# Performance work log

Measured on AMD Instinct MI355X. Metric: run time of the kernel, lower is better.

The kernel has to match this reference:

```python
import jax, jax.numpy as jnp
import numpy as np

N, K, H = 98, 10, 4        # landmarks, neighbors/node, heads
B, CIN, HC = 1024, 256, 64 # batch, in_channels, head_channels
NEG = -9e15


def setup_inputs() -> dict:
    key = jax.random.key(0)
    ks = jax.random.split(key, 3)
    rng = np.random.default_rng(0)
    # fixed sparsity pattern: K unique neighbors per row, row-major order
    cols2d = np.stack([np.sort(rng.choice(N, K, replace=False)) for _ in range(N)])
    rows = np.repeat(np.arange(N), K)
    cols = cols2d.reshape(-1)
    x = jax.random.normal(ks[0], (B, N, CIN), jnp.float32)
    W = jax.random.normal(ks[1], (H, 2, CIN, HC), jnp.float32) * 0.05  # xavier-ish
    e = jnp.ones((H, N * K), jnp.float32)  # nn.init.constant_(e, 1)
    stdv = 1.0 / np.sqrt(HC)
    bias = jax.random.uniform(ks[2], (H, HC), jnp.float32, -stdv, stdv)
    return {"x": x, "W": W, "e": e, "bias": bias,
            "rows": jnp.asarray(rows, jnp.int32),
            "cols": jnp.asarray(cols, jnp.int32)}


def reference(x, W, e, bias, rows, cols):
    # h0/h1 for all heads at once: [2, H, B, N, HC]
    h = jnp.einsum('bnc,hscd->shbnd', x, W)
    h0, h1 = h[0], h[1]
    # masked adjacency logits per head: -9e15 everywhere, learned e at edges
    base = jnp.full((N, N), NEG, jnp.float32)
    logits = jax.vmap(lambda eh: base.at[rows, cols].set(eh))(e)  # [H,N,N]
    A = jax.nn.softmax(logits, axis=-1)  # F.softmax(adj, dim=1) on [N,N]
    diag = jnp.diagonal(A, axis1=-2, axis2=-1)  # [H,N] -> adj*M part
    A_off = A - diag[..., None] * jnp.eye(N, dtype=A.dtype)  # adj*(1-M)
    out = diag[:, None, :, None] * h0 + jnp.einsum('hij,hbjd->hbid', A_off, h1)
    out = out + bias[:, None, None, :]  # [H,B,N,HC]
    # concat heads along channel dim -> [B, N, H*HC]
    return jnp.transpose(out, (1, 2, 0, 3)).reshape(B, N, H * HC)
```

## Files before the change

kernel.cpp:

```cpp
#include <hip/hip_runtime.h>

typedef __bf16 bf16;
typedef bf16 bf16x4 __attribute__((ext_vector_type(4)));
typedef bf16 bf16x8 __attribute__((ext_vector_type(8)));
typedef float f32x4 __attribute__((ext_vector_type(4)));

#define NND 98
#define KNB 10
#define NH 4
#define CIN 256
#define HC 64
#define XROW_B 528
#define CROW_E 136

__global__ __launch_bounds__(256) void prep_wp_kernel(const float* __restrict__ W,
                                                      bf16* __restrict__ Wp) {
  int t = blockIdx.x * 256 + threadIdx.x;
  if (t >= 8 * 8 * 4 * 64) return;
  int lane = t & 63;
  int nt = (t >> 6) & 3;
  int kt = (t >> 8) & 7;
  int hs = t >> 11;
  int n = nt * 16 + (lane & 15);
  int kb = kt * 32 + (lane >> 4) * 8;
  const float* src = W + (hs * CIN + kb) * HC + n;
  bf16x8 v;
#pragma unroll
  for (int j = 0; j < 8; ++j) v[j] = (bf16)src[j * HC];
  *(bf16x8*)(Wp + (long long)t * 8) = v;
}

__global__ __launch_bounds__(1024, 4) void semgconv_kernel(
    const float* __restrict__ x, const float* __restrict__ e,
    const float* __restrict__ bias, const int* __restrict__ cols,
    const bf16* __restrict__ Wp, float* __restrict__ out) {
  __shared__ __align__(16) unsigned char reg0[112 * XROW_B];
  __shared__ float w_lds[NND * KNB];
  __shared__ short cols_lds[NND * KNB];
  __shared__ float diag_lds[NND];

  const int tid = threadIdx.x;
  const int b = blockIdx.x;

  if (tid < NND) {
    const int* cp = cols + tid * KNB;
#pragma unroll
    for (int j = 0; j < KNB; ++j) cols_lds[tid * KNB + j] = (short)cp[j];
  }

  {
    const float* xb = x + (long long)b * NND * CIN;
#pragma unroll
    for (int it = 0; it < 7; ++it) {
      int idx = tid + it * 1024;
      int n = idx >> 6;
      int c4 = (idx & 63) << 2;
      f32x4 v = {0.f, 0.f, 0.f, 0.f};
      if (n < NND) v = *(const f32x4*)(xb + n * CIN + c4);
      bf16x4 bv;
      bv[0] = (bf16)v[0]; bv[1] = (bf16)v[1]; bv[2] = (bf16)v[2]; bv[3] = (bf16)v[3];
      *(bf16x4*)(reg0 + n * XROW_B + c4 * 2) = bv;
    }
  }
  __syncthreads();

  const int lane = tid & 63;
  const int wv = tid >> 6;
  const int wh = wv & 3;
  const int wm = wv >> 2;
  const int mt0 = wm * 2;

  f32x4 acc[2][8] = {};
  const unsigned char* aptr = reg0 + (mt0 * 16 + (lane & 15)) * XROW_B + (lane >> 4) * 16;
  const bf16* wpl = Wp + ((long long)(wh * 2) * (8 * 4 * 64) + lane) * 8;

#pragma unroll
  for (int kt = 0; kt < 8; ++kt) {
    bf16x8 afr[2];
#pragma unroll
    for (int im = 0; im < 2; ++im)
      if (mt0 + im < 7)
        afr[im] = *(const bf16x8*)(aptr + im * (16 * XROW_B) + kt * 64);
    {
      bf16x8 bfr[4];
#pragma unroll
      for (int nt = 0; nt < 4; ++nt)
        bfr[nt] = *(const bf16x8*)(wpl + ((kt * 4 + nt) * 64) * 8);
#pragma unroll
      for (int im = 0; im < 2; ++im)
        if (mt0 + im < 7)
#pragma unroll
          for (int nt = 0; nt < 4; ++nt)
            acc[im][nt] = __builtin_amdgcn_mfma_f32_16x16x32_bf16(afr[im], bfr[nt],
                                                                  acc[im][nt], 0, 0, 0);
    }
    {
      bf16x8 bfr[4];
#pragma unroll
      for (int nt = 0; nt < 4; ++nt)
        bfr[nt] = *(const bf16x8*)(wpl + ((8 * 4 + kt * 4 + nt) * 64) * 8);
#pragma unroll
      for (int im = 0; im < 2; ++im)
        if (mt0 + im < 7)
#pragma unroll
          for (int nt = 0; nt < 4; ++nt)
            acc[im][4 + nt] = __builtin_amdgcn_mfma_f32_16x16x32_bf16(afr[im], bfr[nt],
                                                                      acc[im][4 + nt], 0, 0, 0);
    }
  }
  __syncthreads();

  bf16* C = (bf16*)reg0;
  const int ig = tid >> 4;
  const int d4 = (tid & 15) * 4;

  for (int h = 0; h < NH; ++h) {
    if (tid < NND) {
      const int i = tid;
      const float* ep = e + (h * NND + i) * KNB;
      float ev[KNB];
      float mx = -3.0e38f;
#pragma unroll
      for (int j = 0; j < KNB; ++j) { ev[j] = ep[j]; mx = fmaxf(mx, ev[j]); }
      float s = 0.f;
#pragma unroll
      for (int j = 0; j < KNB; ++j) { ev[j] = __expf(ev[j] - mx); s += ev[j]; }
      const float inv = 1.f / s;
      float dg = 0.f;
#pragma unroll
      for (int j = 0; j < KNB; ++j) {
        float wvv = ev[j] * inv;
        if ((int)cols_lds[i * KNB + j] == i) { dg = wvv; wvv = 0.f; }
        w_lds[i * KNB + j] = wvv;
      }
      diag_lds[i] = dg;
    }
    if (wh == h) {
#pragma unroll
      for (int im = 0; im < 2; ++im) {
        int mt = mt0 + im;
        if (mt < 7) {
          int rowb = mt * 16 + (lane >> 4) * 4;
#pragma unroll
          for (int q = 0; q < 8; ++q) {
            int col = q * 16 + (lane & 15);
#pragma unroll
            for (int r = 0; r < 4; ++r)
              C[(rowb + r) * CROW_E + col] = (bf16)acc[im][q][r];
          }
        }
      }
    }
    __syncthreads();

    {
      f32x4 bs = *(const f32x4*)(bias + h * HC + d4);
      float* outp = out + (long long)b * NND * (NH * HC) + h * HC + d4;
#pragma unroll
      for (int ib = 0; ib < 2; ++ib) {
        int i = ib * 64 + ig;
        if (i < NND) {
          f32x4 av = bs;
          float dg = diag_lds[i];
          bf16x4 c0 = *(const bf16x4*)(C + i * CROW_E + d4);
          av[0] += dg * (float)c0[0];
          av[1] += dg * (float)c0[1];
          av[2] += dg * (float)c0[2];
          av[3] += dg * (float)c0[3];
#pragma unroll
          for (int j = 0; j < KNB; ++j) {
            float wj = w_lds[i * KNB + j];
            int cj = (int)cols_lds[i * KNB + j];
            bf16x4 c1 = *(const bf16x4*)(C + cj * CROW_E + HC + d4);
            av[0] += wj * (float)c1[0];
            av[1] += wj * (float)c1[1];
            av[2] += wj * (float)c1[2];
            av[3] += wj * (float)c1[3];
          }
          *(f32x4*)(outp + (long long)i * (NH * HC)) = av;
        }
      }
    }
    __syncthreads();
  }
}

extern "C" void kernel_launch(void* const* d_in, const int* in_sizes, int n_in,
                              void* d_out, int out_size, void* d_ws, size_t ws_size,
                              hipStream_t stream) {
  const float* x    = (const float*)d_in[0];
  const float* W    = (const float*)d_in[1];
  const float* e    = (const float*)d_in[2];
  const float* bias = (const float*)d_in[3];
  const int* cols   = (const int*)d_in[5];
  float* out        = (float*)d_out;
  bf16* Wp          = (bf16*)d_ws;

  int B = in_sizes[0] / (NND * CIN);

  prep_wp_kernel<<<64, 256, 0, stream>>>(W, Wp);
  semgconv_kernel<<<B, 1024, 0, stream>>>(x, e, bias, cols, Wp, out);
}
```

Measured before the change: 255.5 us.

## Split blocks per (batch, head) and load x directly from global into MFMA fragments

Result: slower. 304.6 us (+19.2%).

```diff
diff --git a/kernel.cpp b/kernel.cpp
--- a/kernel.cpp
+++ b/kernel.cpp
@@ -10,8 +10,7 @@
 #define NH 4
 #define CIN 256
 #define HC 64
-#define XROW_B 528
-#define CROW_E 136
+#define CROW_E 132
 
 __global__ __launch_bounds__(256) void prep_wp_kernel(const float* __restrict__ W,
                                                       bf16* __restrict__ Wp) {
@@ -30,158 +29,135 @@
   *(bf16x8*)(Wp + (long long)t * 8) = v;
 }
 
-__global__ __launch_bounds__(1024, 4) void semgconv_kernel(
+__device__ __forceinline__ bf16x8 load_a8(const float* p) {
+  f32x4 u = *(const f32x4*)p;
+  f32x4 v = *(const f32x4*)(p + 4);
+  bf16x8 a;
+  a[0] = (bf16)u[0]; a[1] = (bf16)u[1]; a[2] = (bf16)u[2]; a[3] = (bf16)u[3];
+  a[4] = (bf16)v[0]; a[5] = (bf16)v[1]; a[6] = (bf16)v[2]; a[7] = (bf16)v[3];
+  return a;
+}
+
+__global__ __launch_bounds__(512, 4) void semgconv_kernel(
     const float* __restrict__ x, const float* __restrict__ e,
     const float* __restrict__ bias, const int* __restrict__ cols,
     const bf16* __restrict__ Wp, float* __restrict__ out) {
-  __shared__ __align__(16) unsigned char reg0[112 * XROW_B];
+  __shared__ __align__(16) bf16 C[112 * CROW_E];
   __shared__ float w_lds[NND * KNB];
   __shared__ short cols_lds[NND * KNB];
   __shared__ float diag_lds[NND];
 
   const int tid = threadIdx.x;
-  const int b = blockIdx.x;
+  const int b = blockIdx.x >> 2;
+  const int h = blockIdx.x & 3;
+
+  const int lane = tid & 63;
+  const int wv = tid >> 6;
+  const int wm = wv & 3;
+  const int sh = wv >> 2;
+  const int mt0 = wm * 2;
+
+  f32x4 acc[2][4] = {};
+  {
+    const float* xb = x + (long long)b * (NND * CIN);
+    const int r0 = mt0 * 16 + (lane & 15);
+    const int kb = (lane >> 4) * 8;
+    const float* ap0 = xb + r0 * CIN + kb;
+    const float* ap1 = ap0 + 16 * CIN;
+    const bool ok0 = (r0 < NND);
+    const bool has1 = (mt0 + 1 < 7);
+    const bf16* wpl = Wp + ((long long)((h * 2 + sh) * 32) * 64 + lane) * 8;
+#pragma unroll
+    for (int kt = 0; kt < 8; ++kt) {
+      bf16x8 afr0 = {}, afr1 = {};
+      if (ok0) afr0 = load_a8(ap0 + kt * 32);
+      if (has1) afr1 = load_a8(ap1 + kt * 32);
+      bf16x8 bfr[4];
+#pragma unroll
+      for (int nt = 0; nt < 4; ++nt)
+        bfr[nt] = *(const bf16x8*)(wpl + (long long)((kt * 4 + nt) * 64) * 8);
+#pragma unroll
+      for (int nt = 0; nt < 4; ++nt)
+        acc[0][nt] = __builtin_amdgcn_mfma_f32_16x16x32_bf16(afr0, bfr[nt], acc[0][nt], 0, 0, 0);
+      if (has1) {
+#pragma unroll
+        for (int nt = 0; nt < 4; ++nt)
+          acc[1][nt] = __builtin_amdgcn_mfma_f32_16x16x32_bf16(afr1, bfr[nt], acc[1][nt], 0, 0, 0);
+      }
+    }
+  }
 
   if (tid < NND) {
-    const int* cp = cols + tid * KNB;
+    const int i = tid;
+    const int* cp = cols + i * KNB;
+    const float* ep = e + (h * NND + i) * KNB;
+    float ev[KNB];
+    int cv[KNB];
+    float mx = -3.0e38f;
 #pragma unroll
-    for (int j = 0; j < KNB; ++j) cols_lds[tid * KNB + j] = (short)cp[j];
+    for (int j = 0; j < KNB; ++j) { cv[j] = cp[j]; ev[j] = ep[j]; mx = fmaxf(mx, ev[j]); }
+    float s = 0.f;
+#pragma unroll
+    for (int j = 0; j < KNB; ++j) { ev[j] = __expf(ev[j] - mx); s += ev[j]; }
+    const float inv = 1.f / s;
+    float dg = 0.f;
+#pragma unroll
+    for (int j = 0; j < KNB; ++j) {
+      float wj = ev[j] * inv;
+      if (cv[j] == i) { dg = wj; wj = 0.f; }
+      w_lds[i * KNB + j] = wj;
+      cols_lds[i * KNB + j] = (short)cv[j];
+    }
+    diag_lds[i] = dg;
   }
 
   {
-    const float* xb = x + (long long)b * NND * CIN;
+    const int rowb = mt0 * 16 + (lane >> 4) * 4;
+    const int colb = sh * 64 + (lane & 15);
 #pragma unroll
-    for (int it = 0; it < 7; ++it) {
-      int idx = tid + it * 1024;
-      int n = idx >> 6;
-      int c4 = (idx & 63) << 2;
-      f32x4 v = {0.f, 0.f, 0.f, 0.f};
-      if (n < NND) v = *(const f32x4*)(xb + n * CIN + c4);
-      bf16x4 bv;
-      bv[0] = (bf16)v[0]; bv[1] = (bf16)v[1]; bv[2] = (bf16)v[2]; bv[3] = (bf16)v[3];
-      *(bf16x4*)(reg0 + n * XROW_B + c4 * 2) = bv;
+    for (int im = 0; im < 2; ++im) {
+      if (mt0 + im < 7) {
+#pragma unroll
+        for (int nt = 0; nt < 4; ++nt) {
+          const int col = colb + nt * 16;
+#pragma unroll
+          for (int r = 0; r < 4; ++r)
+            C[(rowb + im * 16 + r) * CROW_E + col] = (bf16)acc[im][nt][r];
+        }
+      }
     }
   }
   __syncthreads();
 
-  const int lane = tid & 63;
-  const int wv = tid >> 6;
-  const int wh = wv & 3;
-  const int wm = wv >> 2;
-  const int mt0 = wm * 2;
-
-  f32x4 acc[2][8] = {};
-  const unsigned char* aptr = reg0 + (mt0 * 16 + (lane & 15)) * XROW_B + (lane >> 4) * 16;
-  const bf16* wpl = Wp + ((long long)(wh * 2) * (8 * 4 * 64) + lane) * 8;
-
+  {
+    const int d4 = (tid & 15) * 4;
+    const int ig = tid >> 4;
+    f32x4 bs = *(const f32x4*)(bias + h * HC + d4);
+    float* outb = out + (long long)b * (NND * NH * HC) + h * HC + d4;
 #pragma unroll
-  for (int kt = 0; kt < 8; ++kt) {
-    bf16x8 afr[2];
+    for (int p = 0; p < 4; ++p) {
+      const int i = p * 32 + ig;
+      if (i < NND) {
+        f32x4 av = bs;
+        const float dg = diag_lds[i];
+        bf16x4 c0 = *(const bf16x4*)(C + i * CROW_E + d4);
+        av[0] += dg * (float)c0[0];
+        av[1] += dg * (float)c0[1];
+        av[2] += dg * (float)c0[2];
+        av[3] += dg * (float)c0[3];
 #pragma unroll
-    for (int im = 0; im < 2; ++im)
-      if (mt0 + im < 7)
-        afr[im] = *(const bf16x8*)(aptr + im * (16 * XROW_B) + kt * 64);
-    {
-      bf16x8 bfr[4];
-#pragma unroll
-      for (int nt = 0; nt < 4; ++nt)
-        bfr[nt] = *(const bf16x8*)(wpl + ((kt * 4 + nt) * 64) * 8);
-#pragma unroll
-      for (int im = 0; im < 2; ++im)
-        if (mt0 + im < 7)
-#pragma unroll
-          for (int nt = 0; nt < 4; ++nt)
-            acc[im][nt] = __builtin_amdgcn_mfma_f32_16x16x32_bf16(afr[im], bfr[nt],
-                                                                  acc[im][nt], 0, 0, 0);
-    }
-    {
-      bf16x8 bfr[4];
-#pragma unroll
-      for (int nt = 0; nt < 4; ++nt)
-        bfr[nt] = *(const bf16x8*)(wpl + ((8 * 4 + kt * 4 + nt) * 64) * 8);
-#pragma unroll
-      for (int im = 0; im < 2; ++im)
-        if (mt0 + im < 7)
-#pragma unroll
-          for (int nt = 0; nt < 4; ++nt)
-            acc[im][4 + nt] = __builtin_amdgcn_mfma_f32_16x16x32_bf16(afr[im], bfr[nt],
-                                                                      acc[im][4 + nt], 0, 0, 0);
-    }
-  }
-  __syncthreads();
-
-  bf16* C = (bf16*)reg0;
-  const int ig = tid >> 4;
-  const int d4 = (tid & 15) * 4;
-
-  for (int h = 0; h < NH; ++h) {
-    if (tid < NND) {
-      const int i = tid;
-      const float* ep = e + (h * NND + i) * KNB;
-      float ev[KNB];
-      float mx = -3.0e38f;
-#pragma unroll
-      for (int j = 0; j < KNB; ++j) { ev[j] = ep[j]; mx = fmaxf(mx, ev[j]); }
-      float s = 0.f;
-#pragma unroll
-      for (int j = 0; j < KNB; ++j) { ev[j] = __expf(ev[j] - mx); s += ev[j]; }
-      const float inv = 1.f / s;
-      float dg = 0.f;
-#pragma unroll
-      for (int j = 0; j < KNB; ++j) {
-        float wvv = ev[j] * inv;
-        if ((int)cols_lds[i * KNB + j] == i) { dg = wvv; wvv = 0.f; }
-        w_lds[i * KNB + j] = wvv;
-      }
-      diag_lds[i] = dg;
-    }
-    if (wh == h) {
-#pragma unroll
-      for (int im = 0; im < 2; ++im) {
-        int mt = mt0 + im;
-        if (mt < 7) {
-          int rowb = mt * 16 + (lane >> 4) * 4;
-#pragma unroll
-          for (int q = 0; q < 8; ++q) {
-            int col = q * 16 + (lane & 15);
-#pragma unroll
-            for (int r = 0; r < 4; ++r)
-              C[(rowb + r) * CROW_E + col] = (bf16)acc[im][q][r];
-          }
+        for (int j = 0; j < KNB; ++j) {
+          const float wj = w_lds[i * KNB + j];
+          const int cj = cols_lds[i * KNB + j];
+          bf16x4 c1 = *(const bf16x4*)(C + cj * CROW_E + HC + d4);
+          av[0] += wj * (float)c1[0];
+          av[1] += wj * (float)c1[1];
+          av[2] += wj * (float)c1[2];
+          av[3] += wj * (float)c1[3];
         }
+        *(f32x4*)(outb + (long long)i * (NH * HC)) = av;
       }
     }
-    __syncthreads();
-
-    {
-      f32x4 bs = *(const f32x4*)(bias + h * HC + d4);
-      float* outp = out + (long long)b * NND * (NH * HC) + h * HC + d4;
-#pragma unroll
-      for (int ib = 0; ib < 2; ++ib) {
-        int i = ib * 64 + ig;
-        if (i < NND) {
-          f32x4 av = bs;
-          float dg = diag_lds[i];
-          bf16x4 c0 = *(const bf16x4*)(C + i * CROW_E + d4);
-          av[0] += dg * (float)c0[0];
-          av[1] += dg * (float)c0[1];
-          av[2] += dg * (float)c0[2];
-          av[3] += dg * (float)c0[3];
-#pragma unroll
-          for (int j = 0; j < KNB; ++j) {
-            float wj = w_lds[i * KNB + j];
-            int cj = (int)cols_lds[i * KNB + j];
-            bf16x4 c1 = *(const bf16x4*)(C + cj * CROW_E + HC + d4);
-            av[0] += wj * (float)c1[0];
-            av[1] += wj * (float)c1[1];
-            av[2] += wj * (float)c1[2];
-            av[3] += wj * (float)c1[3];
-          }
-          *(f32x4*)(outp + (long long)i * (NH * HC)) = av;
-        }
-      }
-    }
-    __syncthreads();
   }
 }
 
@@ -199,5 +175,5 @@
   int B = in_sizes[0] / (NND * CIN);
 
   prep_wp_kernel<<<64, 256, 0, stream>>>(W, Wp);
-  semgconv_kernel<<<B, 1024, 0, stream>>>(x, e, bias, cols, Wp, out);
+  semgconv_kernel<<<(B * NH), 512, 0, stream>>>(x, e, bias, cols, Wp, out);
 }
```
